# Kernel optimization log

Measured on AMD Instinct MI355X. Metric: run time of the kernel, lower is better.

## Reference

```python
import jax, jax.numpy as jnp
import numpy as np

KERNEL_SIZE = 5
EPS = 1e-6


def setup_inputs() -> dict:
    key = jax.random.key(0)
    k1, k2 = jax.random.split(key)
    b, c, h, w = 16, 512, 64, 64
    hidden = 512
    input_dim = c + KERNEL_SIZE * KERNEL_SIZE  # 537
    x = jax.random.normal(k1, (b, c, h, w), dtype=jnp.float32)
    # 1x1 conv weight, stored as (out, in); kaiming-ish scale
    W = jax.random.normal(k2, (hidden, input_dim), dtype=jnp.float32) * (1.0 / np.sqrt(input_dim))
    bias = jnp.zeros((hidden,), dtype=jnp.float32)
    return {"x": x, "W": W, "bias": bias}


def spatial_descriptor(x, k):
    # x: (b,c,h,w) -> (b, k*k, h, w), local self-similarity (dot product) volume
    b, c, h, w = x.shape
    p = k // 2
    xp = jnp.pad(x, ((0, 0), (0, 0), (p, p), (p, p)))
    # small fixed loop over k*k offsets; each term is a fused multiply-reduce
    corrs = [
        jnp.sum(x * jax.lax.dynamic_slice(xp, (0, 0, di, dj), (b, c, h, w)), axis=1)
        for di in range(k)
        for dj in range(k)
    ]
    return jnp.stack(corrs, axis=1)  # (b, k*k, h, w)


def reference(x, W, bias):
    k = KERNEL_SIZE
    gs = spatial_descriptor(x, k)  # (b, k^2, h, w)
    # featureL2Norm over channel dim (note: eps added to sum-of-squares, then sqrt)
    norm = jnp.sqrt(jnp.sum(gs * gs, axis=1, keepdims=True) + EPS)
    gs = gs / norm
    feat = jnp.concatenate([x, gs], axis=1)  # (b, c+k^2, h, w)
    # 1x1 conv + ReLU
    out = jnp.einsum('bchw,oc->bohw', feat, W) + bias[None, :, None, None]
    return jax.nn.relu(out)
```

## Files before the change

kernel.cpp:

```cpp
#include <hip/hip_runtime.h>
#include <stdint.h>

#define C_IN 512
#define HW 4096
#define NPIX 65536
#define KPAD 544
#define KIN 537
#define HID 512

typedef __attribute__((ext_vector_type(8))) short bf16x8;
typedef __attribute__((ext_vector_type(4))) float f32x4;

__device__ __forceinline__ unsigned short f2bf(float f) {
  union { float f; uint32_t u; } v; v.f = f;
  uint32_t u = v.u;
  return (unsigned short)((u + 0x7fffu + ((u >> 16) & 1u)) >> 16);
}
__device__ __forceinline__ float bf2f(unsigned short h) {
  union { uint32_t u; float f; } v; v.u = ((uint32_t)h) << 16;
  return v.f;
}

__global__ __launch_bounds__(256, 8) void k_prep(const float* __restrict__ x,
                                                 unsigned short* __restrict__ featB,
                                                 const float* __restrict__ W,
                                                 unsigned short* __restrict__ Wb) {
  __shared__ unsigned short sm[64][70];
  int g = blockIdx.x;
  int t = threadIdx.x;
  if (g >= 8192) {
    int idx = (g - 8192) * 256 + t;
    if (idx < HID * KPAD) {
      int o = idx / KPAD;
      int k = idx - o * KPAD;
      float v = (k < KIN) ? W[o * KIN + k] : 0.f;
      Wb[idx] = f2bf(v);
    }
    return;
  }
  int b = g >> 9, cg = (g >> 6) & 7, pt = g & 63;
  int c0 = cg * 64, p0 = pt * 64;
  int lane = t & 63, w = t >> 6;
  const float* xb = x + ((size_t)b * C_IN + c0) * HW + p0;
#pragma unroll
  for (int i = 0; i < 8; ++i) {
    int ch = w * 16 + i * 2;
    float a = xb[(size_t)ch * HW + lane];
    float bq = xb[(size_t)(ch + 1) * HW + lane];
    uint32_t pk = (uint32_t)f2bf(a) | ((uint32_t)f2bf(bq) << 16);
    *(uint32_t*)&sm[lane][ch] = pk;
  }
  __syncthreads();
#pragma unroll
  for (int i = 0; i < 2; ++i) {
    int px = (t >> 3) + i * 32, kg = t & 7;
    int n = b * 4096 + p0 + px;
    *(bf16x8*)(featB + (size_t)n * KPAD + c0 + kg * 8) = *(const bf16x8*)&sm[px][kg * 8];
  }
}

__device__ __forceinline__ int xelem(int sr, int sc, int kg) {
  return (sr * 20 + sc) * 64 + ((kg ^ (sc & 7)) * 8);
}

__global__ __launch_bounds__(256, 8) void k_corr(const unsigned short* __restrict__ featB,
                                                 unsigned short* __restrict__ part) {
  __shared__ unsigned short xt[8 * 20 * 64];
  int g = blockIdx.x;
  int bid = (g & 7) * 1024 + (g >> 3);
  int cs = bid & 7;
  int cg = (bid >> 3) & 3;
  int rg = (bid >> 5) & 15;
  int b  = bid >> 9;
  int t = threadIdx.x;
  int lane = t & 63;
  int w = t >> 6;
  int r0 = rg * 4, c0 = cg * 16;

  bf16x8 v[5];
  int la[5];
#pragma unroll
  for (int i = 0; i < 5; ++i) {
    int flat = t + i * 256;
    int kg = flat & 7, pxi = flat >> 3;
    int sc = pxi % 20, sr = pxi / 20;
    int ir = r0 - 2 + sr, ic = c0 - 2 + sc;
    la[i] = xelem(sr, sc, kg);
    if ((unsigned)ir < 64u && (unsigned)ic < 64u) {
      int n = b * 4096 + ir * 64 + ic;
      v[i] = *(const bf16x8*)(featB + (size_t)n * KPAD + cs * 64 + kg * 8);
    } else {
      v[i] = (bf16x8){0, 0, 0, 0, 0, 0, 0, 0};
    }
  }
#pragma unroll
  for (int i = 0; i < 5; ++i)
    *(bf16x8*)&xt[la[i]] = v[i];
  __syncthreads();

  int i15 = lane & 15;
  int tq = lane >> 4;

  bf16x8 afr[2];
#pragma unroll
  for (int ks = 0; ks < 2; ++ks)
    afr[ks] = *(const bf16x8*)&xt[xelem(w + 2, 2 + i15, ks * 4 + tq)];

  int bBase[2][2];
#pragma unroll
  for (int bi = 0; bi < 2; ++bi)
#pragma unroll
    for (int ks = 0; ks < 2; ++ks)
      bBase[bi][ks] = xelem(w, bi * 4 + i15, ks * 4 + tq);

  int nb = b * 4096 + (r0 + w) * 64 + c0;
  bool take[2][4];
#pragma unroll
  for (int bi = 0; bi < 2; ++bi)
#pragma unroll
    for (int qq = 0; qq < 4; ++qq) {
      int r = 4 * tq + qq;
      int djp = bi * 4 + i15 - r;
      take[bi][qq] = (djp >= 0) && (djp <= 4) && (bi == 0 ? (r <= 7) : (r >= 8));
    }

#pragma unroll 1
  for (int di = 0; di < 5; ++di) {
    unsigned short* pb2 = part + (size_t)(cs * 5 + di) * NPIX * 5 + (size_t)5 * nb;
#pragma unroll
    for (int bi = 0; bi < 2; ++bi) {
      f32x4 acc = (f32x4){0.f, 0.f, 0.f, 0.f};
#pragma unroll
      for (int ks = 0; ks < 2; ++ks) {
        bf16x8 bfr = *(const bf16x8*)&xt[bBase[bi][ks] + di * 1280];
        acc = __builtin_amdgcn_mfma_f32_16x16x32_bf16(afr[ks], bfr, acc, 0, 0, 0);
      }
#pragma unroll
      for (int qq = 0; qq < 4; ++qq)
        if (take[bi][qq])
          pb2[4 * bi + 4 * qq + lane] = f2bf(acc[qq]);
    }
  }
}

__global__ __launch_bounds__(256) void k_norm(const unsigned short* __restrict__ part,
                                              unsigned short* __restrict__ featB) {
  int t = blockIdx.x * 256 + threadIdx.x;
  int n = t >> 2, csh = t & 3;
  float g[25];
#pragma unroll
  for (int k = 0; k < 25; ++k) g[k] = 0.f;
#pragma unroll
  for (int cc = 0; cc < 2; ++cc) {
    int cs = csh * 2 + cc;
#pragma unroll
    for (int di = 0; di < 5; ++di) {
      const unsigned short* pp = part + ((size_t)(cs * 5 + di) * NPIX + n) * 5;
#pragma unroll
      for (int dj = 0; dj < 5; ++dj)
        g[di * 5 + dj] += bf2f(pp[dj]);
    }
  }
#pragma unroll
  for (int k = 0; k < 25; ++k) {
    g[k] += __shfl_xor(g[k], 1);
    g[k] += __shfl_xor(g[k], 2);
  }
  float ss = 0.f;
#pragma unroll
  for (int k = 0; k < 25; ++k) ss += g[k] * g[k];
  float inv = 1.0f / sqrtf(ss + 1e-6f);
  unsigned short buf[8];
#pragma unroll
  for (int j = 0; j < 8; ++j) {
    int k = csh * 8 + j;
    buf[j] = (k < 25) ? f2bf(g[k] * inv) : 0;
  }
  *(bf16x8*)(featB + (size_t)n * KPAD + 512 + csh * 8) = *(bf16x8*)buf;
}

typedef __attribute__((address_space(3))) unsigned int as3_uint;
typedef const __attribute__((address_space(1))) unsigned int as1_uint;

__device__ __forceinline__ void glds16(const void* g, void* l) {
  __builtin_amdgcn_global_load_lds((as1_uint*)g, (as3_uint*)l, 16, 0, 0);
}

__global__ __launch_bounds__(256) void k_gemm(const unsigned short* __restrict__ Wb,
                                              const unsigned short* __restrict__ featB,
                                              const float* __restrict__ bias,
                                              float* __restrict__ out) {
  __shared__ __attribute__((aligned(16))) unsigned short As[2][4096];
  __shared__ __attribute__((aligned(16))) unsigned short Bs[2][4096];
  int g = blockIdx.x;
  int bid = (g & 7) * 256 + (g >> 3);
  int mt = bid & 3;
  int nt = bid >> 2;
  int m0 = mt * 128;
  int n0 = nt * 128;
  int tid = threadIdx.x;
  int wave = tid >> 6;
  int lane = tid & 63;
  int wm = wave >> 1;
  int wn = wave & 1;
  int kg = lane >> 4;

  uint32_t aOff[4], bOff[4];
#pragma unroll
  for (int r = 0; r < 4; ++r) {
    int rr = wm * 64 + r * 16 + (lane & 15);
    aOff[r] = rr * 64 + ((kg ^ ((rr >> 1) & 3)) << 4);
  }
#pragma unroll
  for (int cb = 0; cb < 4; ++cb) {
    int rr = wn * 64 + cb * 16 + (lane & 15);
    bOff[cb] = rr * 64 + ((kg ^ ((rr >> 1) & 3)) << 4);
  }

  f32x4 acc[4][4];
#pragma unroll
  for (int r = 0; r < 4; ++r)
#pragma unroll
    for (int cb = 0; cb < 4; ++cb)
      acc[r][cb] = (f32x4){0.f, 0.f, 0.f, 0.f};

  auto STAGE = [&](int buf, int k0) {
#pragma unroll
    for (int qq = 0; qq < 2; ++qq) {
      int ci = wave * 2 + qq;
      int i = ci * 64 + lane;
      int rr = i >> 2;
      int slot = i & 3;
      int k8 = slot ^ ((rr >> 1) & 3);
      glds16(Wb + (size_t)(m0 + rr) * KPAD + k0 + k8 * 8, (char*)&As[buf][0] + ci * 1024);
      glds16(featB + (size_t)(n0 + rr) * KPAD + k0 + k8 * 8, (char*)&Bs[buf][0] + ci * 1024);
    }
  };

  STAGE(0, 0);
  STAGE(1, 32);
  int cur = 0;
#pragma unroll 1
  for (int t = 0; t < 17; ++t) {
    if (t < 16)
      asm volatile("s_waitcnt vmcnt(4)" ::: "memory");
    else
      asm volatile("s_waitcnt vmcnt(0)" ::: "memory");
    __builtin_amdgcn_s_barrier();
    const char* Ab = (const char*)&As[cur][0];
    const char* Bb = (const char*)&Bs[cur][0];
    bf16x8 af[4], bf[4];
#pragma unroll
    for (int r = 0; r < 4; ++r)
      af[r] = *(const bf16x8*)(Ab + aOff[r]);
#pragma unroll
    for (int cb = 0; cb < 4; ++cb)
      bf[cb] = *(const bf16x8*)(Bb + bOff[cb]);
#pragma unroll
    for (int cb = 0; cb < 4; ++cb)
#pragma unroll
      for (int r = 0; r < 4; ++r)
        acc[r][cb] = __builtin_amdgcn_mfma_f32_16x16x32_bf16(af[r], bf[cb], acc[r][cb], 0, 0, 0);
    __builtin_amdgcn_s_barrier();
    if (t < 15) STAGE(cur, (t + 2) * 32);
    cur ^= 1;
  }

  int bb = n0 >> 12;
  int hwb = n0 & 4095;
  float* outb = out + (size_t)bb * (HID * HW) + hwb;
#pragma unroll
  for (int r = 0; r < 4; ++r) {
    int row0 = m0 + wm * 64 + r * 16 + (lane >> 4) * 4;
    float bv[4];
#pragma unroll
    for (int j = 0; j < 4; ++j) bv[j] = bias[row0 + j];
#pragma unroll
    for (int cb = 0; cb < 4; ++cb) {
      int col = wn * 64 + cb * 16 + (lane & 15);
#pragma unroll
      for (int j = 0; j < 4; ++j) {
        float v2 = acc[r][cb][j] + bv[j];
        v2 = fmaxf(v2, 0.f);
        outb[(size_t)(row0 + j) * HW + col] = v2;
      }
    }
  }
}

extern "C" void kernel_launch(void* const* d_in, const int* in_sizes, int n_in,
                              void* d_out, int out_size, void* d_ws, size_t ws_size,
                              hipStream_t stream) {
  const float* x = (const float*)d_in[0];
  const float* W = (const float*)d_in[1];
  const float* bias = (const float*)d_in[2];
  float* out = (float*)d_out;
  char* ws = (char*)d_ws;
  unsigned short* featB = (unsigned short*)ws;
  unsigned short* Wb = (unsigned short*)(ws + 71303168);
  unsigned short* part = (unsigned short*)(ws + 71860224);

  k_prep<<<9280, 256, 0, stream>>>(x, featB, W, Wb);
  k_corr<<<8192, 256, 0, stream>>>(featB, part);
  k_norm<<<1024, 256, 0, stream>>>(part, featB);
  k_gemm<<<2048, 256, 0, stream>>>(Wb, featB, bias, out);
}
```

Before: 146.4 us.

## Enlarge GEMM tiles to 256x256 with 512 threads and K-step 64

The GEMM moves from 128x128 tiles with 256 threads and K-step 32 to 256x256 tiles with 8 waves and K-step 64. Each wave now holds 8x4 MFMA accumulators, uses a new XOR swizzle for shared memory, and raises wave priority around the MFMA bursts. To fit the larger K-step, the padded K dimension goes from 544 to 576, and the normalisation kernel writes 16-wide chunks. The goal is more data reuse per byte loaded and fewer barrier iterations. In exchange it pads K further, uses much more LDS (likely one block per CU), and launches only 512 blocks, which weakens latency hiding and load balance.

New measurement: 140.5 us. -4.0%, faster.

```diff
diff --git a/kernel.cpp b/kernel.cpp
--- a/kernel.cpp
+++ b/kernel.cpp
@@ -4,7 +4,7 @@
 #define C_IN 512
 #define HW 4096
 #define NPIX 65536
-#define KPAD 544
+#define KPAD 576
 #define KIN 537
 #define HID 512
 
@@ -170,13 +170,15 @@
 #pragma unroll
   for (int k = 0; k < 25; ++k) ss += g[k] * g[k];
   float inv = 1.0f / sqrtf(ss + 1e-6f);
-  unsigned short buf[8];
-#pragma unroll
-  for (int j = 0; j < 8; ++j) {
-    int k = csh * 8 + j;
+  unsigned short buf[16];
+#pragma unroll
+  for (int j = 0; j < 16; ++j) {
+    int k = csh * 16 + j;
     buf[j] = (k < 25) ? f2bf(g[k] * inv) : 0;
   }
-  *(bf16x8*)(featB + (size_t)n * KPAD + 512 + csh * 8) = *(bf16x8*)buf;
+  unsigned short* fb = featB + (size_t)n * KPAD + 512 + csh * 16;
+  *(bf16x8*)(fb) = *(bf16x8*)&buf[0];
+  *(bf16x8*)(fb + 8) = *(bf16x8*)&buf[8];
 }
 
 typedef __attribute__((address_space(3))) unsigned int as3_uint;
@@ -186,101 +188,117 @@
   __builtin_amdgcn_global_load_lds((as1_uint*)g, (as3_uint*)l, 16, 0, 0);
 }
 
-__global__ __launch_bounds__(256) void k_gemm(const unsigned short* __restrict__ Wb,
-                                              const unsigned short* __restrict__ featB,
-                                              const float* __restrict__ bias,
-                                              float* __restrict__ out) {
-  __shared__ __attribute__((aligned(16))) unsigned short As[2][4096];
-  __shared__ __attribute__((aligned(16))) unsigned short Bs[2][4096];
+__global__ __launch_bounds__(512, 2) void k_gemm(const unsigned short* __restrict__ Wb,
+                                                 const unsigned short* __restrict__ featB,
+                                                 const float* __restrict__ bias,
+                                                 float* __restrict__ out) {
+  __shared__ __attribute__((aligned(16))) unsigned short As[2][16384];
+  __shared__ __attribute__((aligned(16))) unsigned short Bs[2][16384];
   int g = blockIdx.x;
-  int bid = (g & 7) * 256 + (g >> 3);
-  int mt = bid & 3;
-  int nt = bid >> 2;
-  int m0 = mt * 128;
-  int n0 = nt * 128;
+  int bid = (g & 7) * 64 + (g >> 3);
+  int mt = bid & 1;
+  int nt = bid >> 1;
+  int m0 = mt * 256;
+  int n0 = nt * 256;
   int tid = threadIdx.x;
   int wave = tid >> 6;
   int lane = tid & 63;
-  int wm = wave >> 1;
-  int wn = wave & 1;
-  int kg = lane >> 4;
-
-  uint32_t aOff[4], bOff[4];
-#pragma unroll
-  for (int r = 0; r < 4; ++r) {
-    int rr = wm * 64 + r * 16 + (lane & 15);
-    aOff[r] = rr * 64 + ((kg ^ ((rr >> 1) & 3)) << 4);
-  }
-#pragma unroll
-  for (int cb = 0; cb < 4; ++cb) {
-    int rr = wn * 64 + cb * 16 + (lane & 15);
-    bOff[cb] = rr * 64 + ((kg ^ ((rr >> 1) & 3)) << 4);
-  }
-
-  f32x4 acc[4][4];
-#pragma unroll
-  for (int r = 0; r < 4; ++r)
-#pragma unroll
-    for (int cb = 0; cb < 4; ++cb)
-      acc[r][cb] = (f32x4){0.f, 0.f, 0.f, 0.f};
+  int wm = wave >> 2;
+  int wn = wave & 3;
+
+  int srow[4], scol[4];
+#pragma unroll
+  for (int i = 0; i < 4; ++i) {
+    uint32_t L = (uint32_t)(i * 512 + tid) * 16;
+    uint32_t Lp = L ^ (((L >> 9) & 1) << 5);
+    srow[i] = Lp >> 7;
+    scol[i] = (Lp >> 4) & 7;
+  }
 
   auto STAGE = [&](int buf, int k0) {
 #pragma unroll
-    for (int qq = 0; qq < 2; ++qq) {
-      int ci = wave * 2 + qq;
-      int i = ci * 64 + lane;
-      int rr = i >> 2;
-      int slot = i & 3;
-      int k8 = slot ^ ((rr >> 1) & 3);
-      glds16(Wb + (size_t)(m0 + rr) * KPAD + k0 + k8 * 8, (char*)&As[buf][0] + ci * 1024);
-      glds16(featB + (size_t)(n0 + rr) * KPAD + k0 + k8 * 8, (char*)&Bs[buf][0] + ci * 1024);
+    for (int i = 0; i < 4; ++i) {
+      char* la = (char*)&As[buf][0] + i * 8192 + wave * 1024;
+      char* lb = (char*)&Bs[buf][0] + i * 8192 + wave * 1024;
+      glds16(Wb + (size_t)(m0 + srow[i]) * KPAD + k0 + scol[i] * 8, la);
+      glds16(featB + (size_t)(n0 + srow[i]) * KPAD + k0 + scol[i] * 8, lb);
     }
   };
 
+  int laneRow = lane & 15;
+  int kswz[2];
+#pragma unroll
+  for (int ks = 0; ks < 2; ++ks)
+    kswz[ks] = (ks * 64 + (lane >> 4) * 16) ^ ((lane & 4) << 3);
+
+  f32x4 acc[8][4];
+#pragma unroll
+  for (int r = 0; r < 8; ++r)
+#pragma unroll
+    for (int c = 0; c < 4; ++c)
+      acc[r][c] = (f32x4){0.f, 0.f, 0.f, 0.f};
+
   STAGE(0, 0);
-  STAGE(1, 32);
-  int cur = 0;
+  STAGE(1, 64);
+  const int NT = 9;
 #pragma unroll 1
-  for (int t = 0; t < 17; ++t) {
-    if (t < 16)
-      asm volatile("s_waitcnt vmcnt(4)" ::: "memory");
+  for (int t = 0; t < NT; ++t) {
+    if (t < NT - 1)
+      asm volatile("s_waitcnt vmcnt(8)" ::: "memory");
     else
       asm volatile("s_waitcnt vmcnt(0)" ::: "memory");
     __builtin_amdgcn_s_barrier();
-    const char* Ab = (const char*)&As[cur][0];
-    const char* Bb = (const char*)&Bs[cur][0];
-    bf16x8 af[4], bf[4];
-#pragma unroll
-    for (int r = 0; r < 4; ++r)
-      af[r] = *(const bf16x8*)(Ab + aOff[r]);
-#pragma unroll
-    for (int cb = 0; cb < 4; ++cb)
-      bf[cb] = *(const bf16x8*)(Bb + bOff[cb]);
-#pragma unroll
-    for (int cb = 0; cb < 4; ++cb)
-#pragma unroll
-      for (int r = 0; r < 4; ++r)
-        acc[r][cb] = __builtin_amdgcn_mfma_f32_16x16x32_bf16(af[r], bf[cb], acc[r][cb], 0, 0, 0);
+    const char* Ab = (const char*)&As[t & 1][0];
+    const char* Bb = (const char*)&Bs[t & 1][0];
+#pragma unroll
+    for (int mh = 0; mh < 2; ++mh) {
+      bf16x8 af[4][2];
+#pragma unroll
+      for (int f = 0; f < 4; ++f)
+#pragma unroll
+        for (int ks = 0; ks < 2; ++ks)
+          af[f][ks] = *(const bf16x8*)(Ab +
+              (wm * 128 + mh * 64 + f * 16 + laneRow) * 128 + kswz[ks]);
+#pragma unroll
+      for (int nh = 0; nh < 2; ++nh) {
+        bf16x8 bf[2][2];
+#pragma unroll
+        for (int nf = 0; nf < 2; ++nf)
+#pragma unroll
+          for (int ks = 0; ks < 2; ++ks)
+            bf[nf][ks] = *(const bf16x8*)(Bb +
+                (wn * 64 + nh * 32 + nf * 16 + laneRow) * 128 + kswz[ks]);
+        __builtin_amdgcn_s_setprio(1);
+#pragma unroll
+        for (int f = 0; f < 4; ++f)
+#pragma unroll
+          for (int nf = 0; nf < 2; ++nf)
+#pragma unroll
+            for (int ks = 0; ks < 2; ++ks)
+              acc[mh * 4 + f][nh * 2 + nf] = __builtin_amdgcn_mfma_f32_16x16x32_bf16(
+                  af[f][ks], bf[nf][ks], acc[mh * 4 + f][nh * 2 + nf], 0, 0, 0);
+        __builtin_amdgcn_s_setprio(0);
+      }
+    }
     __builtin_amdgcn_s_barrier();
-    if (t < 15) STAGE(cur, (t + 2) * 32);
-    cur ^= 1;
+    if (t + 2 < NT) STAGE(t & 1, (t + 2) * 64);
   }
 
   int bb = n0 >> 12;
   int hwb = n0 & 4095;
   float* outb = out + (size_t)bb * (HID * HW) + hwb;
 #pragma unroll
-  for (int r = 0; r < 4; ++r) {
-    int row0 = m0 + wm * 64 + r * 16 + (lane >> 4) * 4;
+  for (int f8 = 0; f8 < 8; ++f8) {
+    int row0 = m0 + wm * 128 + f8 * 16 + (lane >> 4) * 4;
     float bv[4];
 #pragma unroll
     for (int j = 0; j < 4; ++j) bv[j] = bias[row0 + j];
 #pragma unroll
-    for (int cb = 0; cb < 4; ++cb) {
-      int col = wn * 64 + cb * 16 + (lane & 15);
+    for (int c = 0; c < 4; ++c) {
+      int col = wn * 64 + (c >> 1) * 32 + (c & 1) * 16 + (lane & 15);
 #pragma unroll
       for (int j = 0; j < 4; ++j) {
-        float v2 = acc[r][cb][j] + bv[j];
+        float v2 = acc[f8][c][j] + bv[j];
         v2 = fmaxf(v2, 0.f);
         outb[(size_t)(row0 + j) * HW + col] = v2;
       }
@@ -297,11 +315,11 @@
   float* out = (float*)d_out;
   char* ws = (char*)d_ws;
   unsigned short* featB = (unsigned short*)ws;
-  unsigned short* Wb = (unsigned short*)(ws + 71303168);
-  unsigned short* part = (unsigned short*)(ws + 71860224);
-
-  k_prep<<<9280, 256, 0, stream>>>(x, featB, W, Wb);
+  unsigned short* Wb = (unsigned short*)(ws + 75497472);
+  unsigned short* part = (unsigned short*)(ws + 76087296);
+
+  k_prep<<<9344, 256, 0, stream>>>(x, featB, W, Wb);
   k_corr<<<8192, 256, 0, stream>>>(featB, part);
   k_norm<<<1024, 256, 0, stream>>>(part, featB);
-  k_gemm<<<2048, 256, 0, stream>>>(Wb, featB, bias, out);
-}
+  k_gemm<<<512, 512, 0, stream>>>(Wb, featB, bias, out);
+}
```
